# Kernel tuning notes

Hardware: AMD Instinct MI355X
Metric: run time of the kernel (lower is better)

## Reference

```python
import jax, jax.numpy as jnp
import numpy as np
from jax import lax

SIGMA = 1.0          # block_elemnts.combined_sigma
BN_EPS = 1e-5


def setup_inputs() -> dict:
    key = jax.random.key(0)
    k1, k2, k3, k4 = jax.random.split(key, 4)
    B, N, T, C_in, C_out = 8, 1024, 8, 64, 64
    return {
        "points": jax.random.normal(k1, (B, N, 3), dtype=jnp.float32),
        "translations": jax.random.normal(k2, (B, T, 3), dtype=jnp.float32),
        "functions": jax.random.normal(k3, (B, N, C_in), dtype=jnp.float32),
        "k_tensor": jax.random.normal(k4, (C_out, C_in, T), dtype=jnp.float32)
            * np.sqrt(2.0 / (C_in + C_out)),  # xavier_normal_
        "gamma": jnp.ones((C_out,), dtype=jnp.float32),
        "beta": jnp.zeros((C_out,), dtype=jnp.float32),
    }


def reference(points, translations, functions, k_tensor, gamma, beta):
    denom = 2.0 * SIGMA ** 2
    # pairwise squared distances [B,N,N]
    sq = jnp.sum(points * points, axis=-1)                      # [B,N]
    dist = sq[:, :, None] + sq[:, None, :] \
        - 2.0 * jnp.einsum('bnd,bmd->bnm', points, points)      # [B,N,N]
    # interpolation matrix = Gaussian kernel of distances
    interp_rowsum = jnp.sum(jnp.exp(-dist / denom), axis=2, keepdims=True)  # [B,N,1]
    w = functions / interp_rowsum                               # [B,N,Cin]
    # b_tensor[t] = w @ k_tensor[:,:,t]^T  -> [T,B,N,Cout]
    b = jnp.einsum('bnc,oct->tbno', w, k_tensor)
    ptd = jnp.einsum('bnd,btd->tbn', points, translations)      # [T,B,N]
    tsq = jnp.sum(translations * translations, axis=2).T        # [T,B]

    B_, N_, O_ = b.shape[1], b.shape[2], b.shape[3]

    def step(acc, inputs):
        b_t, ptd_t, tsq_t = inputs                              # [B,N,O],[B,N],[B]
        dot = -2.0 * ptd_t                                      # [B,N]
        # exponent = -||p_i - p_j - t||^2 / (2*sigma^2), always <= 0
        q = jnp.exp(-(dist + dot[:, :, None] - dot[:, None, :]
                      + tsq_t[:, None, None]) / denom)          # [B,N,N]
        return acc + jnp.einsum('bnm,bmo->bno', q, b_t), None

    out, _ = lax.scan(step, jnp.zeros((B_, N_, O_), dtype=b.dtype),
                      (b, ptd, tsq))                            # [B,N,O]

    # BatchNorm1d in training mode over (B,N) per channel, then ReLU
    mean = jnp.mean(out, axis=(0, 1))
    var = jnp.var(out, axis=(0, 1))
    xn = (out - mean) * lax.rsqrt(var + BN_EPS) * gamma + beta
    return jax.nn.relu(xn)                                      # [B,N,Cout]
```

## Files before the change

### kernel.cpp

```cpp
#include <hip/hip_runtime.h>
#include <hip/hip_bf16.h>
#include <cstdint>
#include <cstddef>

#define BN_EPS 1e-5f

typedef float f32x4_t __attribute__((ext_vector_type(4)));
typedef __bf16 bf16x8_t __attribute__((ext_vector_type(8)));

__device__ __forceinline__ unsigned short f2bf(float f) {
    __hip_bfloat16 h = __float2bfloat16(f);
    return __builtin_bit_cast(unsigned short, h);
}
__device__ __forceinline__ float bf2f(unsigned short u) {
    unsigned int v = ((unsigned int)u) << 16;
    return __builtin_bit_cast(float, v);
}

__device__ __forceinline__ void gld_lds16(void* lds, const void* gp) {
#if __has_builtin(__builtin_amdgcn_global_load_lds)
    __builtin_amdgcn_global_load_lds(
        (const __attribute__((address_space(1))) unsigned int*)gp,
        (__attribute__((address_space(3))) unsigned int*)lds, 16, 0, 0);
#else
    *(uint4*)lds = *(const uint4*)gp;
#endif
}


__global__ __launch_bounds__(256) void k_g(const float* __restrict__ points,
                                           const float* __restrict__ ktens,
                                           float* __restrict__ rowsum,
                                           unsigned short* __restrict__ kpb,
                                           float* __restrict__ bns) {
    __shared__ float praw[3072];
    __shared__ float px[1024], py[1024], pz[1024], hq[1024];
    __shared__ float part[8][128];
    __shared__ float p2[8][32];

    const int tid = threadIdx.x;
    if (blockIdx.x >= 1024) {
        const int i = (blockIdx.x - 1024) * 256 + tid;
        const int t = i >> 12, o = (i >> 6) & 63, c = i & 63;
        kpb[i] = f2bf(ktens[(o * 64 + c) * 8 + t]);
        if (blockIdx.x == 1024 && tid < 128) bns[tid] = 0.f;
        return;
    }

    const int b  = blockIdx.x & 7;
    const int n0 = (blockIdx.x >> 3) * 8;

    for (int i = tid; i < 3072; i += 256) praw[i] = points[b * 3072 + i];
    __syncthreads();
    for (int n = tid; n < 1024; n += 256) {
        float x = praw[n * 3], y = praw[n * 3 + 1], z = praw[n * 3 + 2];
        px[n] = x; py[n] = y; pz[n] = z;
        hq[n] = -0.5f * (x * x + y * y + z * z);
    }
    __syncthreads();

    const int rhalf = tid >> 7;
    const int c0 = (tid & 127) * 8;
    float vx[8], vy[8], vz[8], vh[8];
    *(float4*)&vx[0] = *(const float4*)&px[c0];
    *(float4*)&vx[4] = *(const float4*)&px[c0 + 4];
    *(float4*)&vy[0] = *(const float4*)&py[c0];
    *(float4*)&vy[4] = *(const float4*)&py[c0 + 4];
    *(float4*)&vz[0] = *(const float4*)&pz[c0];
    *(float4*)&vz[4] = *(const float4*)&pz[c0 + 4];
    *(float4*)&vh[0] = *(const float4*)&hq[c0];
    *(float4*)&vh[4] = *(const float4*)&hq[c0 + 4];

    #pragma unroll
    for (int u = 0; u < 4; ++u) {
        const int rl = u * 2 + rhalf;
        const int row = n0 + rl;
        const float rx = px[row], ry = py[row], rz = pz[row], hr = hq[row];
        float ssum = 0.f;
        #pragma unroll
        for (int j = 0; j < 8; ++j)
            ssum += __expf(hr + vh[j] + rx * vx[j] + ry * vy[j] + rz * vz[j]);
        part[rl][tid & 127] = ssum;
    }
    __syncthreads();
    {
        const int row = tid >> 5, c4l = (tid & 31) * 4;
        float4 p = *(const float4*)&part[row][c4l];
        p2[row][tid & 31] = p.x + p.y + p.z + p.w;
    }
    __syncthreads();
    if (tid < 8) {
        float s = 0.f;
        #pragma unroll
        for (int q = 0; q < 8; ++q) {
            float4 v = *(const float4*)&p2[tid][q * 4];
            s += v.x + v.y + v.z + v.w;
        }
        rowsum[b * 1024 + n0 + tid] = s;
    }
}

__global__ __launch_bounds__(256) void k_prep(const float* __restrict__ points,
                                              const float* __restrict__ trans,
                                              const float* __restrict__ funcs,
                                              const unsigned short* __restrict__ kpb,
                                              const float* __restrict__ rowsum,
                                              unsigned short* __restrict__ bmatT,
                                              float* __restrict__ escale) {
    __shared__ unsigned short Asm[128 * 72];
    __shared__ unsigned short Bsm[128 * 72];
    __shared__ float sfacl[256];

    const int b  = blockIdx.x & 7;
    const int mt = (blockIdx.x >> 3) & 7;
    const int ct = blockIdx.x >> 6;
    const int m0 = mt * 128;

    const int tid  = threadIdx.x;
    const int wave = tid >> 6, lane = tid & 63;
    const int wr = wave >> 1, wc = wave & 1;
    const int fr = lane & 15, quad = lane >> 4;

    {
        const int tloc = tid >> 7, m = tid & 127;
        const int t = ct * 2 + tloc;
        const float tx = trans[b * 24 + t * 3], ty = trans[b * 24 + t * 3 + 1],
                    tz = trans[b * 24 + t * 3 + 2];
        const float* pp = &points[(size_t)(b * 1024 + m0 + m) * 3];
        const float ptd = pp[0] * tx + pp[1] * ty + pp[2] * tz;
        const float tsq = tx * tx + ty * ty + tz * tz;
        const float rsv = rowsum[b * 1024 + m0 + m];
        sfacl[tloc * 128 + m] = __expf(-ptd - 0.5f * tsq) / rsv;
        escale[(size_t)(b * 8 + t) * 1024 + m0 + m] = __expf(ptd);
    }
    #pragma unroll
    for (int rep = 0; rep < 2; ++rep) {
        const int m = rep * 64 + (tid >> 2);
        const int c16 = (tid & 3) * 16;
        const float* fp = &funcs[((size_t)(b * 1024) + m0 + m) * 64 + c16];
        float4 f0 = *(const float4*)fp, f1 = *(const float4*)(fp + 4);
        float4 f2 = *(const float4*)(fp + 8), f3 = *(const float4*)(fp + 12);
        uint4 p0, p1;
        p0.x = f2bf(f0.x) | ((unsigned)f2bf(f0.y) << 16);
        p0.y = f2bf(f0.z) | ((unsigned)f2bf(f0.w) << 16);
        p0.z = f2bf(f1.x) | ((unsigned)f2bf(f1.y) << 16);
        p0.w = f2bf(f1.z) | ((unsigned)f2bf(f1.w) << 16);
        p1.x = f2bf(f2.x) | ((unsigned)f2bf(f2.y) << 16);
        p1.y = f2bf(f2.z) | ((unsigned)f2bf(f2.w) << 16);
        p1.z = f2bf(f3.x) | ((unsigned)f2bf(f3.y) << 16);
        p1.w = f2bf(f3.z) | ((unsigned)f2bf(f3.w) << 16);
        *(uint4*)&Asm[m * 72 + c16] = p0;
        *(uint4*)&Asm[m * 72 + c16 + 8] = p1;
    }
    #pragma unroll
    for (int rep = 0; rep < 4; ++rep) {
        const int col = rep * 32 + (tid >> 3);
        const int c8 = (tid & 7) * 8;
        uint4 v = *(const uint4*)&kpb[(size_t)(ct * 128 + col) * 64 + c8];
        *(uint4*)&Bsm[col * 72 + c8] = v;
    }
    __syncthreads();

    f32x4_t acc[4][4];
    #pragma unroll
    for (int i = 0; i < 4; ++i)
        #pragma unroll
        for (int j = 0; j < 4; ++j) acc[i][j] = f32x4_t{0.f, 0.f, 0.f, 0.f};

    #pragma unroll
    for (int s = 0; s < 2; ++s) {
        uint4 afr[4], bfr[4];
        #pragma unroll
        for (int i = 0; i < 4; ++i)
            afr[i] = *(const uint4*)&Asm[(wr * 64 + i * 16 + fr) * 72 + s * 32 + quad * 8];
        #pragma unroll
        for (int j = 0; j < 4; ++j)
            bfr[j] = *(const uint4*)&Bsm[(wc * 64 + j * 16 + fr) * 72 + s * 32 + quad * 8];
        #pragma unroll
        for (int i = 0; i < 4; ++i)
            #pragma unroll
            for (int j = 0; j < 4; ++j)
                acc[i][j] = __builtin_amdgcn_mfma_f32_16x16x32_bf16(
                    __builtin_bit_cast(bf16x8_t, afr[i]),
                    __builtin_bit_cast(bf16x8_t, bfr[j]),
                    acc[i][j], 0, 0, 0);
    }

    #pragma unroll
    for (int i = 0; i < 4; ++i) {
        #pragma unroll
        for (int j = 0; j < 4; ++j) {
            const int colg = ct * 128 + wc * 64 + j * 16 + fr;
            ushort4 pk;
            {
                const int mb = wr * 64 + i * 16 + quad * 4;
                pk.x = f2bf(acc[i][j][0] * sfacl[wc * 128 + mb + 0]);
                pk.y = f2bf(acc[i][j][1] * sfacl[wc * 128 + mb + 1]);
                pk.z = f2bf(acc[i][j][2] * sfacl[wc * 128 + mb + 2]);
                pk.w = f2bf(acc[i][j][3] * sfacl[wc * 128 + mb + 3]);
                *(ushort4*)&bmatT[(size_t)(b * 512 + colg) * 1024 + m0 + mb] = pk;
            }
        }
    }
}

__global__ __launch_bounds__(256, 2) void k_gemm(const float* __restrict__ points,
                                                 const unsigned short* __restrict__ bmatT,
                                                 const float* __restrict__ escale,
                                                 unsigned short* __restrict__ He2) {
    __shared__ unsigned short Bs[8192];
    __shared__ float escT[1024];
    __shared__ float4 mp[256];

    const int b  = blockIdx.x & 7;
    const int rt = (blockIdx.x >> 3) & 7;
    const int z  = blockIdx.x >> 6;
    const int ogp = z & 1;
    const int kh  = z >> 1;
    const int n0 = rt * 128;
    const int kb = kh * 256;

    const int tid  = threadIdx.x;
    const int wave = tid >> 6, lane = tid & 63;

    {
        const int t = tid >> 5, r4 = (tid & 31) * 4;
        *(float4*)&escT[t * 128 + r4] =
            *(const float4*)&escale[(size_t)(b * 8 + t) * 1024 + n0 + r4];
    }
    {
        const float* pp = &points[(size_t)(b * 1024 + kb + tid) * 3];
        const float x = pp[0], y = pp[1], zz = pp[2];
        mp[tid] = make_float4(x, y, zz, -0.5f * (x * x + y * y + zz * zz));
    }

    const unsigned short* gB = bmatT + (size_t)(b * 512 + ogp * 32) * 1024 + kb;

    const int r16 = lane >> 2;
    const int kq  = lane & 3;
    const int gsw = kq ^ (r16 & 3);

    const int fr = lane & 15;
    const int quad = lane >> 4;
    const int swoff = (quad ^ (fr & 3)) << 4;
    const int row_base = wave * 32;

    float rx0, ry0, rz0, rh0, rx1, ry1, rz1, rh1;
    {
        const float* p0 = &points[(size_t)(b * 1024 + n0 + row_base + fr) * 3];
        rx0 = p0[0]; ry0 = p0[1]; rz0 = p0[2];
        rh0 = -0.5f * (rx0 * rx0 + ry0 * ry0 + rz0 * rz0);
        const float* p1 = &points[(size_t)(b * 1024 + n0 + row_base + 16 + fr) * 3];
        rx1 = p1[0]; ry1 = p1[1]; rz1 = p1[2];
        rh1 = -0.5f * (rx1 * rx1 + ry1 * ry1 + rz1 * rz1);
    }

    f32x4_t acc[2][16];
    #pragma unroll
    for (int i = 0; i < 2; ++i)
        #pragma unroll
        for (int j = 0; j < 16; ++j) acc[i][j] = f32x4_t{0.f, 0.f, 0.f, 0.f};

    for (int kk = 0; kk < 8; ++kk) {
        const int k0 = kk * 32;
        __syncthreads();
        #pragma unroll
        for (int i = 0; i < 4; ++i) {
            const int seg = wave * 4 + i;
            const int t = seg >> 1, oh = (seg & 1) * 16;
            gld_lds16((char*)Bs + seg * 1024 + lane * 16,
                      gB + (size_t)(t * 64 + oh + r16) * 1024 + k0 + gsw * 8);
        }
        uint4 afr0, afr1;
        {
            unsigned short u0[8], u1[8];
            const int mbase = k0 + quad * 8;
            #pragma unroll
            for (int j = 0; j < 8; ++j) {
                const float4 m4 = mp[mbase + j];
                const float e0 = __expf(rh0 + m4.w + rx0 * m4.x + ry0 * m4.y + rz0 * m4.z);
                const float e1 = __expf(rh1 + m4.w + rx1 * m4.x + ry1 * m4.y + rz1 * m4.z);
                u0[j] = f2bf(e0);
                u1[j] = f2bf(e1);
            }
            afr0.x = u0[0] | ((unsigned)u0[1] << 16);
            afr0.y = u0[2] | ((unsigned)u0[3] << 16);
            afr0.z = u0[4] | ((unsigned)u0[5] << 16);
            afr0.w = u0[6] | ((unsigned)u0[7] << 16);
            afr1.x = u1[0] | ((unsigned)u1[1] << 16);
            afr1.y = u1[2] | ((unsigned)u1[3] << 16);
            afr1.z = u1[4] | ((unsigned)u1[5] << 16);
            afr1.w = u1[6] | ((unsigned)u1[7] << 16);
        }
        __syncthreads();
        #pragma unroll
        for (int j = 0; j < 16; ++j) {
            uint4 bfr = *(const uint4*)((const char*)Bs + (j * 16 + fr) * 64 + swoff);
            acc[0][j] = __builtin_amdgcn_mfma_f32_16x16x32_bf16(
                __builtin_bit_cast(bf16x8_t, afr0),
                __builtin_bit_cast(bf16x8_t, bfr), acc[0][j], 0, 0, 0);
            acc[1][j] = __builtin_amdgcn_mfma_f32_16x16x32_bf16(
                __builtin_bit_cast(bf16x8_t, afr1),
                __builtin_bit_cast(bf16x8_t, bfr), acc[1][j], 0, 0, 0);
        }
    }

    const int oo = lane & 15;
    unsigned short* dst = He2 + (size_t)kh * 524288
                              + (size_t)(b * 1024 + n0) * 64 + ogp * 32;
    #pragma unroll
    for (int i = 0; i < 2; ++i) {
        #pragma unroll
        for (int r = 0; r < 4; ++r) {
            const int row = row_base + i * 16 + quad * 4 + r;
            float s0 = 0.f, s1 = 0.f;
            #pragma unroll
            for (int t = 0; t < 8; ++t) {
                const float e = escT[t * 128 + row];
                s0 += e * acc[i][2 * t][r];
                s1 += e * acc[i][2 * t + 1][r];
            }
            dst[(size_t)row * 64 + oo] = f2bf(s0);
            dst[(size_t)row * 64 + 16 + oo] = f2bf(s1);
        }
    }
}

__global__ __launch_bounds__(256) void k_fin(const unsigned short* __restrict__ He2,
                                             float* __restrict__ out,
                                             float* __restrict__ bns) {
    __shared__ float s1[16][64], s2[16][64];
    const int tid = threadIdx.x;
    float a0 = 0.f, a1 = 0.f, a2 = 0.f, a3 = 0.f;
    float q0 = 0.f, q1 = 0.f, q2 = 0.f, q3 = 0.f;
    #pragma unroll
    for (int it = 0; it < 2; ++it) {
        const size_t idx = (size_t)blockIdx.x * 512 + it * 256 + tid;
        float4 s = make_float4(0.f, 0.f, 0.f, 0.f);
        #pragma unroll
        for (int p = 0; p < 4; ++p) {
            ushort4 u = *(const ushort4*)(He2 + (size_t)p * 524288 + idx * 4);
            s.x += bf2f(u.x); s.y += bf2f(u.y); s.z += bf2f(u.z); s.w += bf2f(u.w);
        }
        ((float4*)out)[idx] = s;
        a0 += s.x; a1 += s.y; a2 += s.z; a3 += s.w;
        q0 += s.x * s.x; q1 += s.y * s.y; q2 += s.z * s.z; q3 += s.w * s.w;
    }
    const int g = tid >> 4, o4 = (tid & 15) * 4;
    *(float4*)&s1[g][o4] = make_float4(a0, a1, a2, a3);
    *(float4*)&s2[g][o4] = make_float4(q0, q1, q2, q3);
    __syncthreads();
    if (tid < 64) {
        float sa = 0.f, sb = 0.f;
        #pragma unroll
        for (int r = 0; r < 16; ++r) { sa += s1[r][tid]; sb += s2[r][tid]; }
        atomicAdd(&bns[tid], sa);
        atomicAdd(&bns[64 + tid], sb);
    }
}

__global__ __launch_bounds__(256) void k_bn(float* __restrict__ out,
                                            const float* __restrict__ bns,
                                            const float* __restrict__ gamma,
                                            const float* __restrict__ beta) {
    const int i = blockIdx.x * 256 + threadIdx.x;
    const int o4 = (i & 15) * 4;
    float4 x = ((float4*)out)[i];
    const float4 s  = *(const float4*)&bns[o4];
    const float4 s2 = *(const float4*)&bns[64 + o4];
    const float4 gm = *(const float4*)&gamma[o4];
    const float4 bt = *(const float4*)&beta[o4];
    const float invn = 1.f / 8192.f;
    float m, v, w;
    m = s.x * invn; v = s2.x * invn - m * m; w = __frsqrt_rn(v + BN_EPS) * gm.x;
    x.x = fmaxf((x.x - m) * w + bt.x, 0.f);
    m = s.y * invn; v = s2.y * invn - m * m; w = __frsqrt_rn(v + BN_EPS) * gm.y;
    x.y = fmaxf((x.y - m) * w + bt.y, 0.f);
    m = s.z * invn; v = s2.z * invn - m * m; w = __frsqrt_rn(v + BN_EPS) * gm.z;
    x.z = fmaxf((x.z - m) * w + bt.z, 0.f);
    m = s.w * invn; v = s2.w * invn - m * m; w = __frsqrt_rn(v + BN_EPS) * gm.w;
    x.w = fmaxf((x.w - m) * w + bt.w, 0.f);
    ((float4*)out)[i] = x;
}

extern "C" void kernel_launch(void* const* d_in, const int* in_sizes, int n_in,
                              void* d_out, int out_size, void* d_ws, size_t ws_size,
                              hipStream_t stream) {
    const float* points = (const float*)d_in[0];
    const float* trans  = (const float*)d_in[1];
    const float* funcs  = (const float*)d_in[2];
    const float* ktens  = (const float*)d_in[3];
    const float* gamma  = (const float*)d_in[4];
    const float* beta   = (const float*)d_in[5];
    float* out = (float*)d_out;

    float* ws      = (float*)d_ws;
    float* escale  = ws;
    float* bns     = escale + 65536;
    float* rowsum  = bns + 128;
    unsigned short* He2   = (unsigned short*)(rowsum + 8192);
    unsigned short* kpb   = He2 + 2097152;
    unsigned short* bmatT = kpb + 32768;

    k_g<<<1152, 256, 0, stream>>>(points, ktens, rowsum, kpb, bns);
    k_prep<<<256, 256, 0, stream>>>(points, trans, funcs, kpb, rowsum, bmatT, escale);
    k_gemm<<<512, 256, 0, stream>>>(points, bmatT, escale, He2);
    k_fin<<<256, 256, 0, stream>>>(He2, out, bns);
    k_bn<<<512, 256, 0, stream>>>(out, bns, gamma, beta);
}
```

Before: 106.2 us.

## Merge rowsum and prep kernels, fold rowsum into gemm exponent

The rowsum kernel and the weight-prep GEMM kernel become one launch with block-index dispatch and a shared-memory union. The prep GEMM no longer depends on rowsum: the 1/rowsum factor is folded into the main GEMM's per-point exponent as -log(rowsum), so the two can run concurrently. The k_tensor transpose to bf16 now happens inside each prep block, and rowsum blocks each cover 16 rows instead of 8. k_fin and k_bn also get remapped block indices, presumably for better memory locality. The cost is a log per point, strided k_tensor reads, and a small numerical change from moving the division into the exponent.

```diff
diff --git a/kernel.cpp b/kernel.cpp
--- a/kernel.cpp
+++ b/kernel.cpp
@@ -28,27 +28,147 @@
 }
 
 
-__global__ __launch_bounds__(256) void k_g(const float* __restrict__ points,
-                                           const float* __restrict__ ktens,
-                                           float* __restrict__ rowsum,
-                                           unsigned short* __restrict__ kpb,
-                                           float* __restrict__ bns) {
-    __shared__ float praw[3072];
-    __shared__ float px[1024], py[1024], pz[1024], hq[1024];
-    __shared__ float part[8][128];
-    __shared__ float p2[8][32];
-
+union SmemGP {
+    struct {
+        float praw[3072];
+        float px[1024], py[1024], pz[1024], hq[1024];
+        float part[16][128];
+        float p2[16][32];
+    } g;
+    struct {
+        unsigned short Asm[128 * 72];
+        unsigned short Bsm[128 * 72];
+        float sfacl[256];
+    } p;
+};
+
+__global__ __launch_bounds__(256) void k_gp(const float* __restrict__ points,
+                                            const float* __restrict__ trans,
+                                            const float* __restrict__ funcs,
+                                            const float* __restrict__ ktens,
+                                            float* __restrict__ rowsum,
+                                            unsigned short* __restrict__ bmatT,
+                                            float* __restrict__ escale,
+                                            float* __restrict__ bns) {
+    __shared__ SmemGP smu;
     const int tid = threadIdx.x;
-    if (blockIdx.x >= 1024) {
-        const int i = (blockIdx.x - 1024) * 256 + tid;
-        const int t = i >> 12, o = (i >> 6) & 63, c = i & 63;
-        kpb[i] = f2bf(ktens[(o * 64 + c) * 8 + t]);
-        if (blockIdx.x == 1024 && tid < 128) bns[tid] = 0.f;
+
+    if (blockIdx.x >= 512) {
+        const int bk = blockIdx.x - 512;
+        const int b  = bk & 7;
+        const int mt = (bk >> 3) & 7;
+        const int ct = bk >> 6;
+        const int m0 = mt * 128;
+
+        unsigned short* Asm = smu.p.Asm;
+        unsigned short* Bsm = smu.p.Bsm;
+        float* sfacl = smu.p.sfacl;
+
+        if (blockIdx.x == 512 && tid < 128) bns[tid] = 0.f;
+
+        const int wave = tid >> 6, lane = tid & 63;
+        const int wr = wave >> 1, wc = wave & 1;
+        const int fr = lane & 15, quad = lane >> 4;
+
+        {
+            const int tloc = tid >> 7, m = tid & 127;
+            const int t = ct * 2 + tloc;
+            const float tx = trans[b * 24 + t * 3], ty = trans[b * 24 + t * 3 + 1],
+                        tz = trans[b * 24 + t * 3 + 2];
+            const float* pp = &points[(size_t)(b * 1024 + m0 + m) * 3];
+            const float ptd = pp[0] * tx + pp[1] * ty + pp[2] * tz;
+            const float tsq = tx * tx + ty * ty + tz * tz;
+            sfacl[tloc * 128 + m] = __expf(-ptd - 0.5f * tsq);
+            escale[(size_t)(b * 8 + t) * 1024 + m0 + m] = __expf(ptd);
+        }
+        #pragma unroll
+        for (int rep = 0; rep < 2; ++rep) {
+            const int m = rep * 64 + (tid >> 2);
+            const int c16 = (tid & 3) * 16;
+            const float* fp = &funcs[((size_t)(b * 1024) + m0 + m) * 64 + c16];
+            float4 f0 = *(const float4*)fp, f1 = *(const float4*)(fp + 4);
+            float4 f2 = *(const float4*)(fp + 8), f3 = *(const float4*)(fp + 12);
+            uint4 p0, p1;
+            p0.x = f2bf(f0.x) | ((unsigned)f2bf(f0.y) << 16);
+            p0.y = f2bf(f0.z) | ((unsigned)f2bf(f0.w) << 16);
+            p0.z = f2bf(f1.x) | ((unsigned)f2bf(f1.y) << 16);
+            p0.w = f2bf(f1.z) | ((unsigned)f2bf(f1.w) << 16);
+            p1.x = f2bf(f2.x) | ((unsigned)f2bf(f2.y) << 16);
+            p1.y = f2bf(f2.z) | ((unsigned)f2bf(f2.w) << 16);
+            p1.z = f2bf(f3.x) | ((unsigned)f2bf(f3.y) << 16);
+            p1.w = f2bf(f3.z) | ((unsigned)f2bf(f3.w) << 16);
+            *(uint4*)&Asm[m * 72 + c16] = p0;
+            *(uint4*)&Asm[m * 72 + c16 + 8] = p1;
+        }
+        #pragma unroll
+        for (int rep = 0; rep < 4; ++rep) {
+            const int col = rep * 32 + (tid >> 3);
+            const int c8  = (tid & 7) * 8;
+            const int g   = ct * 128 + col;
+            const int t   = g >> 6, o = g & 63;
+            const float* kt = &ktens[(size_t)(o * 64 + c8) * 8 + t];
+            unsigned short us[8];
+            #pragma unroll
+            for (int q = 0; q < 8; ++q) us[q] = f2bf(kt[q * 8]);
+            uint4 v;
+            v.x = us[0] | ((unsigned)us[1] << 16);
+            v.y = us[2] | ((unsigned)us[3] << 16);
+            v.z = us[4] | ((unsigned)us[5] << 16);
+            v.w = us[6] | ((unsigned)us[7] << 16);
+            *(uint4*)&Bsm[col * 72 + c8] = v;
+        }
+        __syncthreads();
+
+        f32x4_t acc[4][4];
+        #pragma unroll
+        for (int i = 0; i < 4; ++i)
+            #pragma unroll
+            for (int j = 0; j < 4; ++j) acc[i][j] = f32x4_t{0.f, 0.f, 0.f, 0.f};
+
+        #pragma unroll
+        for (int s = 0; s < 2; ++s) {
+            uint4 afr[4], bfr[4];
+            #pragma unroll
+            for (int i = 0; i < 4; ++i)
+                afr[i] = *(const uint4*)&Asm[(wr * 64 + i * 16 + fr) * 72 + s * 32 + quad * 8];
+            #pragma unroll
+            for (int j = 0; j < 4; ++j)
+                bfr[j] = *(const uint4*)&Bsm[(wc * 64 + j * 16 + fr) * 72 + s * 32 + quad * 8];
+            #pragma unroll
+            for (int i = 0; i < 4; ++i)
+                #pragma unroll
+                for (int j = 0; j < 4; ++j)
+                    acc[i][j] = __builtin_amdgcn_mfma_f32_16x16x32_bf16(
+                        __builtin_bit_cast(bf16x8_t, afr[i]),
+                        __builtin_bit_cast(bf16x8_t, bfr[j]),
+                        acc[i][j], 0, 0, 0);
+        }
+
+        #pragma unroll
+        for (int i = 0; i < 4; ++i) {
+            #pragma unroll
+            for (int j = 0; j < 4; ++j) {
+                const int colg = ct * 128 + wc * 64 + j * 16 + fr;
+                ushort4 pk;
+                const int mb = wr * 64 + i * 16 + quad * 4;
+                pk.x = f2bf(acc[i][j][0] * sfacl[wc * 128 + mb + 0]);
+                pk.y = f2bf(acc[i][j][1] * sfacl[wc * 128 + mb + 1]);
+                pk.z = f2bf(acc[i][j][2] * sfacl[wc * 128 + mb + 2]);
+                pk.w = f2bf(acc[i][j][3] * sfacl[wc * 128 + mb + 3]);
+                *(ushort4*)&bmatT[(size_t)(b * 512 + colg) * 1024 + m0 + mb] = pk;
+            }
+        }
         return;
     }
 
+    float* praw = smu.g.praw;
+    float* px = smu.g.px; float* py = smu.g.py;
+    float* pz = smu.g.pz; float* hq = smu.g.hq;
+    float (*part)[128] = smu.g.part;
+    float (*p2)[32] = smu.g.p2;
+
     const int b  = blockIdx.x & 7;
-    const int n0 = (blockIdx.x >> 3) * 8;
+    const int n0 = (blockIdx.x >> 3) * 16;
 
     for (int i = tid; i < 3072; i += 256) praw[i] = points[b * 3072 + i];
     __syncthreads();
@@ -72,7 +192,7 @@
     *(float4*)&vh[4] = *(const float4*)&hq[c0 + 4];
 
     #pragma unroll
-    for (int u = 0; u < 4; ++u) {
+    for (int u = 0; u < 8; ++u) {
         const int rl = u * 2 + rhalf;
         const int row = n0 + rl;
         const float rx = px[row], ry = py[row], rz = pz[row], hr = hq[row];
@@ -83,13 +203,14 @@
         part[rl][tid & 127] = ssum;
     }
     __syncthreads();
-    {
-        const int row = tid >> 5, c4l = (tid & 31) * 4;
+    #pragma unroll
+    for (int rep = 0; rep < 2; ++rep) {
+        const int row = rep * 8 + (tid >> 5), c4l = (tid & 31) * 4;
         float4 p = *(const float4*)&part[row][c4l];
         p2[row][tid & 31] = p.x + p.y + p.z + p.w;
     }
     __syncthreads();
-    if (tid < 8) {
+    if (tid < 16) {
         float s = 0.f;
         #pragma unroll
         for (int q = 0; q < 8; ++q) {
@@ -100,113 +221,10 @@
     }
 }
 
-__global__ __launch_bounds__(256) void k_prep(const float* __restrict__ points,
-                                              const float* __restrict__ trans,
-                                              const float* __restrict__ funcs,
-                                              const unsigned short* __restrict__ kpb,
-                                              const float* __restrict__ rowsum,
-                                              unsigned short* __restrict__ bmatT,
-                                              float* __restrict__ escale) {
-    __shared__ unsigned short Asm[128 * 72];
-    __shared__ unsigned short Bsm[128 * 72];
-    __shared__ float sfacl[256];
-
-    const int b  = blockIdx.x & 7;
-    const int mt = (blockIdx.x >> 3) & 7;
-    const int ct = blockIdx.x >> 6;
-    const int m0 = mt * 128;
-
-    const int tid  = threadIdx.x;
-    const int wave = tid >> 6, lane = tid & 63;
-    const int wr = wave >> 1, wc = wave & 1;
-    const int fr = lane & 15, quad = lane >> 4;
-
-    {
-        const int tloc = tid >> 7, m = tid & 127;
-        const int t = ct * 2 + tloc;
-        const float tx = trans[b * 24 + t * 3], ty = trans[b * 24 + t * 3 + 1],
-                    tz = trans[b * 24 + t * 3 + 2];
-        const float* pp = &points[(size_t)(b * 1024 + m0 + m) * 3];
-        const float ptd = pp[0] * tx + pp[1] * ty + pp[2] * tz;
-        const float tsq = tx * tx + ty * ty + tz * tz;
-        const float rsv = rowsum[b * 1024 + m0 + m];
-        sfacl[tloc * 128 + m] = __expf(-ptd - 0.5f * tsq) / rsv;
-        escale[(size_t)(b * 8 + t) * 1024 + m0 + m] = __expf(ptd);
-    }
-    #pragma unroll
-    for (int rep = 0; rep < 2; ++rep) {
-        const int m = rep * 64 + (tid >> 2);
-        const int c16 = (tid & 3) * 16;
-        const float* fp = &funcs[((size_t)(b * 1024) + m0 + m) * 64 + c16];
-        float4 f0 = *(const float4*)fp, f1 = *(const float4*)(fp + 4);
-        float4 f2 = *(const float4*)(fp + 8), f3 = *(const float4*)(fp + 12);
-        uint4 p0, p1;
-        p0.x = f2bf(f0.x) | ((unsigned)f2bf(f0.y) << 16);
-        p0.y = f2bf(f0.z) | ((unsigned)f2bf(f0.w) << 16);
-        p0.z = f2bf(f1.x) | ((unsigned)f2bf(f1.y) << 16);
-        p0.w = f2bf(f1.z) | ((unsigned)f2bf(f1.w) << 16);
-        p1.x = f2bf(f2.x) | ((unsigned)f2bf(f2.y) << 16);
-        p1.y = f2bf(f2.z) | ((unsigned)f2bf(f2.w) << 16);
-        p1.z = f2bf(f3.x) | ((unsigned)f2bf(f3.y) << 16);
-        p1.w = f2bf(f3.z) | ((unsigned)f2bf(f3.w) << 16);
-        *(uint4*)&Asm[m * 72 + c16] = p0;
-        *(uint4*)&Asm[m * 72 + c16 + 8] = p1;
-    }
-    #pragma unroll
-    for (int rep = 0; rep < 4; ++rep) {
-        const int col = rep * 32 + (tid >> 3);
-        const int c8 = (tid & 7) * 8;
-        uint4 v = *(const uint4*)&kpb[(size_t)(ct * 128 + col) * 64 + c8];
-        *(uint4*)&Bsm[col * 72 + c8] = v;
-    }
-    __syncthreads();
-
-    f32x4_t acc[4][4];
-    #pragma unroll
-    for (int i = 0; i < 4; ++i)
-        #pragma unroll
-        for (int j = 0; j < 4; ++j) acc[i][j] = f32x4_t{0.f, 0.f, 0.f, 0.f};
-
-    #pragma unroll
-    for (int s = 0; s < 2; ++s) {
-        uint4 afr[4], bfr[4];
-        #pragma unroll
-        for (int i = 0; i < 4; ++i)
-            afr[i] = *(const uint4*)&Asm[(wr * 64 + i * 16 + fr) * 72 + s * 32 + quad * 8];
-        #pragma unroll
-        for (int j = 0; j < 4; ++j)
-            bfr[j] = *(const uint4*)&Bsm[(wc * 64 + j * 16 + fr) * 72 + s * 32 + quad * 8];
-        #pragma unroll
-        for (int i = 0; i < 4; ++i)
-            #pragma unroll
-            for (int j = 0; j < 4; ++j)
-                acc[i][j] = __builtin_amdgcn_mfma_f32_16x16x32_bf16(
-                    __builtin_bit_cast(bf16x8_t, afr[i]),
-                    __builtin_bit_cast(bf16x8_t, bfr[j]),
-                    acc[i][j], 0, 0, 0);
-    }
-
-    #pragma unroll
-    for (int i = 0; i < 4; ++i) {
-        #pragma unroll
-        for (int j = 0; j < 4; ++j) {
-            const int colg = ct * 128 + wc * 64 + j * 16 + fr;
-            ushort4 pk;
-            {
-                const int mb = wr * 64 + i * 16 + quad * 4;
-                pk.x = f2bf(acc[i][j][0] * sfacl[wc * 128 + mb + 0]);
-                pk.y = f2bf(acc[i][j][1] * sfacl[wc * 128 + mb + 1]);
-                pk.z = f2bf(acc[i][j][2] * sfacl[wc * 128 + mb + 2]);
-                pk.w = f2bf(acc[i][j][3] * sfacl[wc * 128 + mb + 3]);
-                *(ushort4*)&bmatT[(size_t)(b * 512 + colg) * 1024 + m0 + mb] = pk;
-            }
-        }
-    }
-}
-
 __global__ __launch_bounds__(256, 2) void k_gemm(const float* __restrict__ points,
                                                  const unsigned short* __restrict__ bmatT,
                                                  const float* __restrict__ escale,
+                                                 const float* __restrict__ rowsum,
                                                  unsigned short* __restrict__ He2) {
     __shared__ unsigned short Bs[8192];
     __shared__ float escT[1024];
@@ -231,7 +249,9 @@
     {
         const float* pp = &points[(size_t)(b * 1024 + kb + tid) * 3];
         const float x = pp[0], y = pp[1], zz = pp[2];
-        mp[tid] = make_float4(x, y, zz, -0.5f * (x * x + y * y + zz * zz));
+        const float rs = rowsum[b * 1024 + kb + tid];
+        mp[tid] = make_float4(x, y, zz,
+                              -0.5f * (x * x + y * y + zz * zz) - __logf(rs));
     }
 
     const unsigned short* gB = bmatT + (size_t)(b * 512 + ogp * 32) * 1024 + kb;
@@ -331,11 +351,12 @@
                                              float* __restrict__ bns) {
     __shared__ float s1[16][64], s2[16][64];
     const int tid = threadIdx.x;
+    const int vb = ((blockIdx.x & 7) << 5) | (blockIdx.x >> 3);
     float a0 = 0.f, a1 = 0.f, a2 = 0.f, a3 = 0.f;
     float q0 = 0.f, q1 = 0.f, q2 = 0.f, q3 = 0.f;
     #pragma unroll
     for (int it = 0; it < 2; ++it) {
-        const size_t idx = (size_t)blockIdx.x * 512 + it * 256 + tid;
+        const size_t idx = (size_t)vb * 512 + it * 256 + tid;
         float4 s = make_float4(0.f, 0.f, 0.f, 0.f);
         #pragma unroll
         for (int p = 0; p < 4; ++p) {
@@ -363,7 +384,8 @@
                                             const float* __restrict__ bns,
                                             const float* __restrict__ gamma,
                                             const float* __restrict__ beta) {
-    const int i = blockIdx.x * 256 + threadIdx.x;
+    const int vb = ((blockIdx.x & 7) << 6) | (blockIdx.x >> 3);
+    const int i = vb * 256 + threadIdx.x;
     const int o4 = (i & 15) * 4;
     float4 x = ((float4*)out)[i];
     const float4 s  = *(const float4*)&bns[o4];
@@ -399,12 +421,11 @@
     float* bns     = escale + 65536;
     float* rowsum  = bns + 128;
     unsigned short* He2   = (unsigned short*)(rowsum + 8192);
-    unsigned short* kpb   = He2 + 2097152;
-    unsigned short* bmatT = kpb + 32768;
-
-    k_g<<<1152, 256, 0, stream>>>(points, ktens, rowsum, kpb, bns);
-    k_prep<<<256, 256, 0, stream>>>(points, trans, funcs, kpb, rowsum, bmatT, escale);
-    k_gemm<<<512, 256, 0, stream>>>(points, bmatT, escale, He2);
+    unsigned short* bmatT = He2 + 2097152;
+
+    k_gp<<<768, 256, 0, stream>>>(points, trans, funcs, ktens,
+                                  rowsum, bmatT, escale, bns);
+    k_gemm<<<512, 256, 0, stream>>>(points, bmatT, escale, rowsum, He2);
     k_fin<<<256, 256, 0, stream>>>(He2, out, bns);
     k_bn<<<512, 256, 0, stream>>>(out, bns, gamma, beta);
 }
```

After: 103.1 us. -2.9%, faster.
